# Kernel tuning notes

Measured on AMD Instinct MI355X. Metric: run time of the kernel, lower is better.

The kernel has to match this reference:

```python
import jax, jax.numpy as jnp
import numpy as np

B = 65536      # batch
E = 4          # experts per node
F = 32         # per-node input features
H = 256        # hidden width
NODES = 4
D_MID = 128    # intermediate node output dim
D_OUT = 8      # final head dim


def _lin_w(k, fan_in, fan_out):
    b = 1.0 / np.sqrt(fan_in)
    return jax.random.uniform(k, (E, fan_in, fan_out), jnp.float32, -b, b)


def setup_inputs() -> dict:
    key = jax.random.key(0)
    ks = jax.random.split(key, 8)
    feats = jax.random.normal(ks[0], (B, NODES * F), dtype=jnp.float32)
    # routing one-hot blocks embedded in the input vector (as the module expects)
    ohs = [jax.nn.one_hot(jax.random.randint(ks[1 + j], (B,), 0, E), E, dtype=jnp.float32)
           for j in range(NODES)]
    input_val = jnp.concatenate([feats] + ohs, axis=1)  # [B, 144]
    p = {"input_val": input_val}
    kc = iter(jax.random.split(ks[5], 32))
    # node 0: no pre-interface; post: F->H relu, H->D_MID relu
    p["W0_0"] = _lin_w(next(kc), F, H); p["b0_0"] = jnp.full((E, H), 0.1, jnp.float32)
    p["W0_1"] = _lin_w(next(kc), H, D_MID); p["b0_1"] = jnp.full((E, D_MID), 0.1, jnp.float32)
    # nodes 1,2: pre F->H relu; post (D_MID+H)->H relu, H->D_MID relu
    for j in (1, 2):
        p[f"W{j}_pre"] = _lin_w(next(kc), F, H); p[f"b{j}_pre"] = jnp.full((E, H), 0.1, jnp.float32)
        p[f"W{j}_0"] = _lin_w(next(kc), D_MID + H, H); p[f"b{j}_0"] = jnp.full((E, H), 0.1, jnp.float32)
        p[f"W{j}_1"] = _lin_w(next(kc), H, D_MID); p[f"b{j}_1"] = jnp.full((E, D_MID), 0.1, jnp.float32)
    # node 3 (output): pre F->H relu; post (D_MID+H)->H relu, H->D_OUT identity
    p["W3_pre"] = _lin_w(next(kc), F, H); p["b3_pre"] = jnp.full((E, H), 0.1, jnp.float32)
    p["W3_0"] = _lin_w(next(kc), D_MID + H, H); p["b3_0"] = jnp.full((E, H), 0.1, jnp.float32)
    p["W3_1"] = jax.random.uniform(next(kc), (E, H, D_OUT), jnp.float32, -0.003, 0.003)
    p["b3_1"] = jax.random.uniform(next(kc), (E, D_OUT), jnp.float32, -0.003, 0.003)
    return p


def reference(input_val, W0_0, b0_0, W0_1, b0_1,
              W1_pre, b1_pre, W1_0, b1_0, W1_1, b1_1,
              W2_pre, b2_pre, W2_0, b2_0, W2_1, b2_1,
              W3_pre, b3_pre, W3_0, b3_0, W3_1, b3_1):
    relu = jax.nn.relu
    xs = [input_val[:, j * F:(j + 1) * F] for j in range(NODES)]          # per-node features
    ohs = [input_val[:, NODES * F + j * E: NODES * F + (j + 1) * E] for j in range(NODES)]

    def combine(oh, outs):  # oh [B,E] exact one-hot; outs [E,B,D] -> exact per-row expert pick
        return jnp.einsum('be,ebo->bo', oh, outs)

    # node 0 (no previous-level input)
    def n0(W0, b0, W1, b1):
        h = relu(xs[0] @ W0 + b0)
        return relu(h @ W1 + b1)
    x = combine(ohs[0], jax.vmap(n0)(W0_0, b0_0, W0_1, b0_1))  # [B, D_MID]

    def node(xj, xprev, relu_last):
        def f(Wp, bp, W0, b0, W1, b1):
            h = relu(xj @ Wp + bp)                      # pre-interface
            h = jnp.concatenate([xprev, h], axis=-1)    # interface: cat(prev, pre)
            h = relu(h @ W0 + b0)
            o = h @ W1 + b1
            return relu(o) if relu_last else o
        return f

    x = combine(ohs[1], jax.vmap(node(xs[1], x, True))(W1_pre, b1_pre, W1_0, b1_0, W1_1, b1_1))
    x = combine(ohs[2], jax.vmap(node(xs[2], x, True))(W2_pre, b2_pre, W2_0, b2_0, W2_1, b2_1))
    x = combine(ohs[3], jax.vmap(node(xs[3], x, False))(W3_pre, b3_pre, W3_0, b3_0, W3_1, b3_1))
    return x  # [B, D_OUT]
```

## Files before the change

### kernel.cpp

```cpp
#include <hip/hip_runtime.h>
#include <hip/hip_bf16.h>
#include <stdint.h>

typedef unsigned int u32;
typedef unsigned short u16;
typedef unsigned char u8;
typedef __bf16 bf16x8 __attribute__((ext_vector_type(8)));
typedef float f32x4 __attribute__((ext_vector_type(4)));

#define NB 65536
#define NBLK 1280
#define PERM_TOT (NBLK * 64)
#define INVR 0xFFFFFFFFu
#define BLK_DEAD 0xFFFFu

#define O_ROWS 0
#define O_XJ   256
#define O_P    (O_XJ + 4096)
#define O_H    (O_P + 16384)
#define O_RED  O_P
#define SM_BYTES (O_H + 32768)

__device__ __host__ constexpr int TS(int m) {
  constexpr int t[12] = {0, 64, 320, 384, 1152, 1408, 1472, 2240, 2496, 2560, 3328, 3360};
  return t[m];
}

__device__ __forceinline__ u16 f2bf(float f) {
  u32 u = __builtin_bit_cast(u32, f);
  u32 r = (u + 0x7FFFu + ((u >> 16) & 1u)) >> 16;
  return (u16)r;
}
__device__ __forceinline__ u32 cvtpk(float lo, float hi) {
  u32 r;
  asm("v_cvt_pk_bf16_f32 %0, %1, %2" : "=v"(r) : "v"(lo), "v"(hi));
  return r;
}
__device__ __forceinline__ float relu_f(float x) { return x > 0.f ? x : 0.f; }
__device__ __forceinline__ f32x4 mfma16(bf16x8 a, bf16x8 b, f32x4 c) {
  return __builtin_amdgcn_mfma_f32_16x16x32_bf16(a, b, c, 0, 0, 0);
}

__device__ __forceinline__ void mkpair(f32x4 acc, float bias, bool dorelu, int l16,
                                       u32& w0, u32& w1) {
  float v0 = acc[0] + bias, v1 = acc[1] + bias, v2 = acc[2] + bias, v3 = acc[3] + bias;
  if (dorelu) { v0 = relu_f(v0); v1 = relu_f(v1); v2 = relu_f(v2); v3 = relu_f(v3); }
  u32 a = cvtpk(v0, v1);
  u32 b = cvtpk(v2, v3);
  u32 ax = (u32)__shfl_xor((int)a, 1);
  u32 bx = (u32)__shfl_xor((int)b, 1);
  if ((l16 & 1) == 0) { w0 = (a & 0xffffu) | (ax << 16); w1 = (a >> 16) | (ax & 0xffff0000u); }
  else                { w0 = (bx & 0xffffu) | (b << 16); w1 = (bx >> 16) | (b & 0xffff0000u); }
}

__device__ __forceinline__ void frag_store_pair(char* base, int KT, int m0, int col,
                                                u32 w0, u32 w1) {
  char* d = base + (((m0 >> 4) * KT + (col >> 5)) << 10) +
            (((m0 & 15) + (((col & 31) >> 3) << 4)) << 4) + (col & 7) * 2;
  *(u32*)d = w0; *(u32*)(d + 16) = w1;
}


struct PrepArgs {
  const float* src[11];
  int K[11], Nsrc[11];
  int tileStart[12];
};

__device__ __forceinline__ void prep_tile_dev(__bf16* __restrict__ pk, const PrepArgs& pa,
                                              int gt, int lane) {
  const int quad = lane >> 4, l16 = lane & 15;
  int m = 0;
  while (gt >= pa.tileStart[m + 1]) m++;
  const int loc = gt - pa.tileStart[m];
  const int K = pa.K[m], Ns = pa.Nsrc[m];
  const int Np = Ns < 16 ? 16 : Ns;
  const int KT = K >> 5, NT = Np >> 4;
  const int e = loc / (KT * NT), rem = loc % (KT * NT);
  const int nt = rem / KT, kt = rem % KT;
  const int k = kt * 32 + quad * 8, n = nt * 16 + l16;
  u32 hw[4];
  if (n < Ns) {
    const float* s = pa.src[m] + ((size_t)e * K + k) * Ns + n;
    u16 h[8];
#pragma unroll
    for (int j = 0; j < 8; j++) h[j] = f2bf(s[(size_t)j * Ns]);
    hw[0] = (u32)h[0] | ((u32)h[1] << 16);
    hw[1] = (u32)h[2] | ((u32)h[3] << 16);
    hw[2] = (u32)h[4] | ((u32)h[5] << 16);
    hw[3] = (u32)h[6] | ((u32)h[7] << 16);
  } else {
    hw[0] = hw[1] = hw[2] = hw[3] = 0u;
  }
  uint4 w; w.x = hw[0]; w.y = hw[1]; w.z = hw[2]; w.w = hw[3];
  *(uint4*)((char*)pk + (size_t)gt * 1024 + lane * 16) = w;
}


__global__ __launch_bounds__(256) void k_front(const float* __restrict__ inp,
                                               u8* __restrict__ bkt,
                                               u32* __restrict__ cnt2,
                                               u32* __restrict__ rank,
                                               __bf16* __restrict__ pk, PrepArgs pa) {
  __shared__ u32 h[256];
  const int tid = threadIdx.x;
  if (blockIdx.x == 0) rank[tid] = 0u;
  h[tid] = 0u;
  __syncthreads();
  const int r = blockIdx.x * 256 + tid;
  const float4* oh = (const float4*)(inp + (size_t)r * 144 + 128);
  u32 b = 0;
#pragma unroll
  for (int j = 0; j < 4; j++) {
    float4 v = oh[j];
    u32 e = v.y > 0.5f ? 1u : (v.z > 0.5f ? 2u : (v.w > 0.5f ? 3u : 0u));
    b |= e << (2 * j);
  }
  bkt[r] = (u8)b;
  atomicAdd(&h[b], 1u);
  __syncthreads();
  cnt2[blockIdx.x * 256 + tid] = h[tid];
  for (int g4 = blockIdx.x; g4 < TS(11) / 4; g4 += 256)
    prep_tile_dev(pk, pa, g4 * 4 + (tid >> 6), tid & 63);
}


__global__ __launch_bounds__(256) void k_place(const u8* __restrict__ bkt,
                                               const u32* __restrict__ cnt2,
                                               u32* __restrict__ rank,
                                               u16* __restrict__ blk2b,
                                               u32* __restrict__ perm) {
  __shared__ u32 s[256], base[256];
  const int tid = threadIdx.x;
  u32 c = 0;
#pragma unroll 8
  for (int j = 0; j < 256; j++) c += cnt2[j * 256 + tid];
  const u32 pad = (c + 63u) & ~63u;
  s[tid] = pad;
  __syncthreads();
  for (int d = 1; d < 256; d <<= 1) {
    u32 v = (tid >= d) ? s[tid - d] : 0u;
    __syncthreads();
    s[tid] += v;
    __syncthreads();
  }
  const u32 off = s[tid] - pad;
  const u32 total = s[255];
  __syncthreads();
  if (blockIdx.x == 0) {
    for (u32 i = off + c; i < off + pad; i++) perm[i] = INVR;
    for (u32 blk = off >> 6; blk < (off + pad) >> 6; blk++) blk2b[blk] = (u16)tid;
    for (u32 blk = (total >> 6) + tid; blk < NBLK; blk += 256) blk2b[blk] = BLK_DEAD;
  }
  s[tid] = 0u;
  __syncthreads();
  const int r = blockIdx.x * 256 + tid;
  const u32 b = bkt[r];
  const u32 lrk = atomicAdd(&s[b], 1u);
  __syncthreads();
  base[tid] = off + (s[tid] ? atomicAdd(&rank[tid], s[tid]) : 0u);
  __syncthreads();
  perm[base[b] + lrk] = (u32)r;
}


__device__ __forceinline__ void xj_load(const float* inp, u32 myrow, int tid, int node,
                                        float4& v0, float4& v1) {
  v0 = make_float4(0.f, 0.f, 0.f, 0.f); v1 = v0;
  if (tid < 256 && myrow != INVR) {
    const int c8 = (tid & 3) << 3;
    const float4* p = (const float4*)(inp + (size_t)myrow * 144 + node * 32 + c8);
    v0 = p[0]; v1 = p[1];
  }
}

__device__ __forceinline__ void xj_store(char* sm, int tid, float4 v0, float4 v1) {
  if (tid >= 256) return;
  const int r = tid >> 2;
  uint4 w;
  w.x = cvtpk(v0.x, v0.y);
  w.y = cvtpk(v0.z, v0.w);
  w.z = cvtpk(v1.x, v1.y);
  w.w = cvtpk(v1.z, v1.w);
  *(uint4*)(sm + O_XJ + ((r >> 4) << 10) + ((((tid & 3) << 4) + (r & 15)) << 4)) = w;
}

__device__ __forceinline__ void pre_gemm(char* sm, u32 e, int wave, int lane,
                                         const __bf16* Wp, const float* bp) {
  const int l16 = lane & 15;
  const int wn0 = wave * 32;
  const int rsel = ((lane >> 4) << 2) + ((l16 & 1) ? 2 : 0);
  const int colp = l16 & ~1;
  float bias[2];
#pragma unroll
  for (int nt = 0; nt < 2; nt++) bias[nt] = bp[(size_t)e * 256 + wn0 + nt * 16 + l16];
  f32x4 acc[4][2];
#pragma unroll
  for (int i = 0; i < 4; i++) { acc[i][0] = (f32x4){0.f,0.f,0.f,0.f}; acc[i][1] = acc[i][0]; }
  bf16x8 a[4], b[2];
#pragma unroll
  for (int nt = 0; nt < 2; nt++)
    b[nt] = *(const bf16x8*)(Wp + (size_t)(e * 16 + (wn0 >> 4) + nt) * 512 + lane * 8);
#pragma unroll
  for (int mt = 0; mt < 4; mt++)
    a[mt] = *(const bf16x8*)(sm + O_XJ + (mt << 10) + lane * 16);
#pragma unroll
  for (int mt = 0; mt < 4; mt++)
#pragma unroll
    for (int nt = 0; nt < 2; nt++) acc[mt][nt] = mfma16(a[mt], b[nt], acc[mt][nt]);
#pragma unroll
  for (int nt = 0; nt < 2; nt++) {
    const int n = wn0 + nt * 16;
#pragma unroll
    for (int mt = 0; mt < 4; mt++) {
      u32 w0, w1;
      mkpair(acc[mt][nt], bias[nt], true, l16, w0, w1);
      frag_store_pair(sm + O_H, 8, mt * 16 + rsel, n + colp, w0, w1);
    }
  }
}

__device__ __forceinline__ void main_gemm(char* sm, u32 e, int wave, int lane,
                                          const __bf16* Wm, const float* bm) {
  const int l16 = lane & 15;
  const int wn0 = wave * 32;
  const int rsel = ((lane >> 4) << 2) + ((l16 & 1) ? 2 : 0);
  const int colp = l16 & ~1;
  float bias[2];
#pragma unroll
  for (int nt = 0; nt < 2; nt++) bias[nt] = bm[(size_t)e * 256 + wn0 + nt * 16 + l16];
  f32x4 acc[4][2];
#pragma unroll
  for (int i = 0; i < 4; i++) { acc[i][0] = (f32x4){0.f,0.f,0.f,0.f}; acc[i][1] = acc[i][0]; }
  const __bf16* bB = Wm + (size_t)(e * 16 + (wn0 >> 4)) * 12 * 512 + lane * 8;
  bf16x8 bb[2][2];
#pragma unroll
  for (int nt = 0; nt < 2; nt++) {
    bb[0][nt] = *(const bf16x8*)(bB + (size_t)(nt * 12 + 0) * 512);
    bb[1][nt] = *(const bf16x8*)(bB + (size_t)(nt * 12 + 1) * 512);
  }
#pragma unroll
  for (int kt = 0; kt < 12; kt++) {
    bf16x8 a[4];
#pragma unroll
    for (int mt = 0; mt < 4; mt++) {
      a[mt] = (kt < 4)
          ? *(const bf16x8*)(sm + O_P + ((mt * 4 + kt) << 10) + lane * 16)
          : *(const bf16x8*)(sm + O_H + ((mt * 8 + (kt - 4)) << 10) + lane * 16);
    }
#pragma unroll
    for (int mt = 0; mt < 4; mt++)
#pragma unroll
      for (int nt = 0; nt < 2; nt++) acc[mt][nt] = mfma16(a[mt], bb[kt & 1][nt], acc[mt][nt]);
    if (kt < 10) {
#pragma unroll
      for (int nt = 0; nt < 2; nt++)
        bb[kt & 1][nt] = *(const bf16x8*)(bB + (size_t)(nt * 12 + kt + 2) * 512);
    }
  }
  __syncthreads();
#pragma unroll
  for (int nt = 0; nt < 2; nt++) {
    const int n = wn0 + nt * 16;
#pragma unroll
    for (int mt = 0; mt < 4; mt++) {
      u32 w0, w1;
      mkpair(acc[mt][nt], bias[nt], true, l16, w0, w1);
      frag_store_pair(sm + O_H, 8, mt * 16 + rsel, n + colp, w0, w1);
    }
  }
  __syncthreads();
}

__device__ __forceinline__ void out_gemm(char* sm, u32 e, int wave, int lane,
                                         const __bf16* Wo, const float* bo) {
  const int l16 = lane & 15;
  const int on0 = wave * 16;
  const int rsel = ((lane >> 4) << 2) + ((l16 & 1) ? 2 : 0);
  const int colp = l16 & ~1;
  const float bias0 = bo[(size_t)e * 128 + on0 + l16];
  f32x4 acc[4];
#pragma unroll
  for (int i = 0; i < 4; i++) acc[i] = (f32x4){0.f, 0.f, 0.f, 0.f};
  const __bf16* bB = Wo + (size_t)(e * 8 + (on0 >> 4)) * 8 * 512 + lane * 8;
  bf16x8 bb[2];
  bb[0] = *(const bf16x8*)(bB);
  bb[1] = *(const bf16x8*)(bB + 512);
#pragma unroll
  for (int kt = 0; kt < 8; kt++) {
    bf16x8 a[4];
#pragma unroll
    for (int mt = 0; mt < 4; mt++)
      a[mt] = *(const bf16x8*)(sm + O_H + ((mt * 8 + kt) << 10) + lane * 16);
#pragma unroll
    for (int mt = 0; mt < 4; mt++) acc[mt] = mfma16(a[mt], bb[kt & 1], acc[mt]);
    if (kt < 6) bb[kt & 1] = *(const bf16x8*)(bB + (size_t)(kt + 2) * 512);
  }
#pragma unroll
  for (int mt = 0; mt < 4; mt++) {
    u32 w0, w1;
    mkpair(acc[mt], bias0, true, l16, w0, w1);
    frag_store_pair(sm + O_P, 4, mt * 16 + rsel, on0 + colp, w0, w1);
  }
}

__global__ __launch_bounds__(512, 6) void fused_k(
    const float* __restrict__ inp, const u32* __restrict__ perm,
    const u16* __restrict__ blk2b, const __bf16* __restrict__ pk,
    const float* __restrict__ b0_0, const float* __restrict__ b0_1,
    const float* __restrict__ b1_p, const float* __restrict__ b1_0,
    const float* __restrict__ b1_1, const float* __restrict__ b2_p,
    const float* __restrict__ b2_0, const float* __restrict__ b2_1,
    const float* __restrict__ b3_p, const float* __restrict__ b3_0,
    const float* __restrict__ b3_1, float* __restrict__ dout) {
  const u32 b = blk2b[blockIdx.x];
  if (b == BLK_DEAD) return;
  __shared__ __align__(16) char sm[SM_BYTES];
  u32* rows = (u32*)sm;
  const int tid = threadIdx.x;
  const int wave = tid >> 6, lane = tid & 63, quad = lane >> 4, l16 = lane & 15;
  if (tid < 64) rows[tid] = perm[blockIdx.x * 64 + tid];
  const u32 e0 = b & 3u, e1 = (b >> 2) & 3u, e2 = (b >> 4) & 3u, e3 = (b >> 6) & 3u;
  __syncthreads();
  const u32 myrow = rows[(tid & 255) >> 2];

  float4 v0, v1;
  xj_load(inp, myrow, tid, 0, v0, v1);
  xj_store(sm, tid, v0, v1);
  __syncthreads();
  pre_gemm(sm, e0, wave, lane, pk + (size_t)TS(0) * 512, b0_0);
  __syncthreads();
  xj_load(inp, myrow, tid, 1, v0, v1);
  out_gemm(sm, e0, wave, lane, pk + (size_t)TS(1) * 512, b0_1);
  xj_store(sm, tid, v0, v1);
  __syncthreads();
  pre_gemm(sm, e1, wave, lane, pk + (size_t)TS(2) * 512, b1_p);
  __syncthreads();
  main_gemm(sm, e1, wave, lane, pk + (size_t)TS(3) * 512, b1_0);
  xj_load(inp, myrow, tid, 2, v0, v1);
  out_gemm(sm, e1, wave, lane, pk + (size_t)TS(4) * 512, b1_1);
  xj_store(sm, tid, v0, v1);
  __syncthreads();
  pre_gemm(sm, e2, wave, lane, pk + (size_t)TS(5) * 512, b2_p);
  __syncthreads();
  main_gemm(sm, e2, wave, lane, pk + (size_t)TS(6) * 512, b2_0);
  xj_load(inp, myrow, tid, 3, v0, v1);
  out_gemm(sm, e2, wave, lane, pk + (size_t)TS(7) * 512, b2_1);
  xj_store(sm, tid, v0, v1);
  __syncthreads();
  pre_gemm(sm, e3, wave, lane, pk + (size_t)TS(8) * 512, b3_p);
  __syncthreads();
  main_gemm(sm, e3, wave, lane, pk + (size_t)TS(9) * 512, b3_0);

  {
    const __bf16* Wo3 = pk + (size_t)TS(10) * 512;
    if (wave < 4) {
      f32x4 acc3[4];
#pragma unroll
      for (int i = 0; i < 4; i++) acc3[i] = (f32x4){0.f, 0.f, 0.f, 0.f};
#pragma unroll
      for (int kk = 0; kk < 2; kk++) {
        const int kt = wave * 2 + kk;
        bf16x8 b3 = *(const bf16x8*)(Wo3 + (size_t)(e3 * 8 + kt) * 512 + lane * 8);
        bf16x8 a[4];
#pragma unroll
        for (int mt = 0; mt < 4; mt++)
          a[mt] = *(const bf16x8*)(sm + O_H + ((mt * 8 + kt) << 10) + lane * 16);
#pragma unroll
        for (int mt = 0; mt < 4; mt++) acc3[mt] = mfma16(a[mt], b3, acc3[mt]);
      }
#pragma unroll
      for (int mt = 0; mt < 4; mt++)
#pragma unroll
        for (int r = 0; r < 4; r++)
          *(float*)(sm + O_RED +
                    (((size_t)wave * 64 + mt * 16 + quad * 4 + r) * 16 + l16) * 4) = acc3[mt][r];
    }
    __syncthreads();
    if (tid < 256) {
      const int m = tid >> 2, c = (tid & 3) * 2;
      float s0 = 0.f, s1 = 0.f;
#pragma unroll
      for (int w = 0; w < 4; w++) {
        s0 += *(float*)(sm + O_RED + (((size_t)w * 64 + m) * 16 + c) * 4);
        s1 += *(float*)(sm + O_RED + (((size_t)w * 64 + m) * 16 + c + 1) * 4);
      }
      if (myrow != INVR) {
        float2 o;
        o.x = s0 + b3_1[(size_t)e3 * 8 + c];
        o.y = s1 + b3_1[(size_t)e3 * 8 + c + 1];
        *(float2*)(dout + (size_t)myrow * 8 + c) = o;
      }
    }
  }
}


extern "C" void kernel_launch(void* const* d_in, const int* in_sizes, int n_in,
                              void* d_out, int out_size, void* d_ws, size_t ws_size,
                              hipStream_t stream) {
  (void)in_sizes; (void)n_in; (void)out_size; (void)ws_size;
  const float* inp = (const float*)d_in[0];
  char* ws = (char*)d_ws;

  const size_t oBKT = 0;
  const size_t oRANK = oBKT + NB;
  const size_t oB2B = oRANK + 1024;
  const size_t oCNT2 = (oB2B + NBLK * 2 + 255) & ~(size_t)255;
  const size_t oPERM = oCNT2 + 256 * 256 * 4;
  const size_t oPK = (oPERM + (size_t)PERM_TOT * 4 + 255) & ~(size_t)255;

  u8* bkt = (u8*)(ws + oBKT);
  u32* rank = (u32*)(ws + oRANK);
  u16* blk2b = (u16*)(ws + oB2B);
  u32* cnt2 = (u32*)(ws + oCNT2);
  u32* perm = (u32*)(ws + oPERM);
  __bf16* pk = (__bf16*)(ws + oPK);

  PrepArgs pa;
  const int widx[11] = {1, 3, 5, 7, 9, 11, 13, 15, 17, 19, 21};
  const int Ks[11] = {32, 256, 32, 384, 256, 32, 384, 256, 32, 384, 256};
  const int Ns[11] = {256, 128, 256, 256, 128, 256, 256, 128, 256, 256, 8};
  for (int m = 0; m < 11; m++) {
    pa.src[m] = (const float*)d_in[widx[m]];
    pa.K[m] = Ks[m]; pa.Nsrc[m] = Ns[m]; pa.tileStart[m] = TS(m);
  }
  pa.tileStart[11] = TS(11);

  hipLaunchKernelGGL(k_front, dim3(NB / 256), dim3(256), 0, stream,
                     inp, bkt, cnt2, rank, pk, pa);
  hipLaunchKernelGGL(k_place, dim3(NB / 256), dim3(256), 0, stream,
                     bkt, cnt2, rank, blk2b, perm);
  fused_k<<<NBLK, 512, 0, stream>>>(
      inp, perm, blk2b, pk,
      (const float*)d_in[2], (const float*)d_in[4],
      (const float*)d_in[6], (const float*)d_in[8], (const float*)d_in[10],
      (const float*)d_in[12], (const float*)d_in[14], (const float*)d_in[16],
      (const float*)d_in[18], (const float*)d_in[20], (const float*)d_in[22],
      (float*)d_out);
}
```

Measured before the change: 215.3 us.

## Pre-convert features to bf16 in front kernel and stage via direct global-to-LDS loads

The front kernel now converts all 128 feature columns of every row to bf16 and writes them to a workspace buffer. The fused kernel then copies each node's 32-column slice straight into shared memory with global_load_lds, run by four waves, in place of fp32 loads followed by register conversion and LDS stores. This halves the bytes gathered per row in the main kernel and removes the conversion and store instructions from its critical path. The cost is an extra full pass over the input plus a write of a B×128 bf16 buffer in the front kernel.

```diff
diff --git a/kernel.cpp b/kernel.cpp
--- a/kernel.cpp
+++ b/kernel.cpp
@@ -101,6 +101,7 @@
                                                u8* __restrict__ bkt,
                                                u32* __restrict__ cnt2,
                                                u32* __restrict__ rank,
+                                               u32* __restrict__ fb_u32,
                                                __bf16* __restrict__ pk, PrepArgs pa) {
   __shared__ u32 h[256];
   const int tid = threadIdx.x;
@@ -120,6 +121,15 @@
   atomicAdd(&h[b], 1u);
   __syncthreads();
   cnt2[blockIdx.x * 256 + tid] = h[tid];
+#pragma unroll 4
+  for (int it = 0; it < 32; it++) {
+    const int cg = it * 256 + tid;
+    const int lrow = cg >> 5, c4 = cg & 31;
+    const size_t grow = (size_t)blockIdx.x * 256 + lrow;
+    float4 v = *(const float4*)(inp + grow * 144 + c4 * 4);
+    uint2 o; o.x = cvtpk(v.x, v.y); o.y = cvtpk(v.z, v.w);
+    *(uint2*)(fb_u32 + grow * 64 + c4 * 2) = o;
+  }
   for (int g4 = blockIdx.x; g4 < TS(11) / 4; g4 += 256)
     prep_tile_dev(pk, pa, g4 * 4 + (tid >> 6), tid & 63);
 }
@@ -164,25 +174,14 @@
 }
 
 
-__device__ __forceinline__ void xj_load(const float* inp, u32 myrow, int tid, int node,
-                                        float4& v0, float4& v1) {
-  v0 = make_float4(0.f, 0.f, 0.f, 0.f); v1 = v0;
-  if (tid < 256 && myrow != INVR) {
-    const int c8 = (tid & 3) << 3;
-    const float4* p = (const float4*)(inp + (size_t)myrow * 144 + node * 32 + c8);
-    v0 = p[0]; v1 = p[1];
-  }
-}
-
-__device__ __forceinline__ void xj_store(char* sm, int tid, float4 v0, float4 v1) {
-  if (tid >= 256) return;
-  const int r = tid >> 2;
-  uint4 w;
-  w.x = cvtpk(v0.x, v0.y);
-  w.y = cvtpk(v0.z, v0.w);
-  w.z = cvtpk(v1.x, v1.y);
-  w.w = cvtpk(v1.z, v1.w);
-  *(uint4*)(sm + O_XJ + ((r >> 4) << 10) + ((((tid & 3) << 4) + (r & 15)) << 4)) = w;
+__device__ __forceinline__ void xj_stage(char* sm, const __bf16* fbsrc, int node,
+                                         int wave) {
+  if (wave < 4) {
+    __builtin_amdgcn_global_load_lds(
+        (const __attribute__((address_space(1))) void*)(fbsrc + node * 32),
+        (__attribute__((address_space(3))) void*)(sm + O_XJ + (wave << 10)),
+        16, 0, 0);
+  }
 }
 
 __device__ __forceinline__ void pre_gemm(char* sm, u32 e, int wave, int lane,
@@ -305,7 +304,7 @@
 }
 
 __global__ __launch_bounds__(512, 6) void fused_k(
-    const float* __restrict__ inp, const u32* __restrict__ perm,
+    const __bf16* __restrict__ fb, const u32* __restrict__ perm,
     const u16* __restrict__ blk2b, const __bf16* __restrict__ pk,
     const float* __restrict__ b0_0, const float* __restrict__ b0_1,
     const float* __restrict__ b1_p, const float* __restrict__ b1_0,
@@ -322,31 +321,31 @@
   if (tid < 64) rows[tid] = perm[blockIdx.x * 64 + tid];
   const u32 e0 = b & 3u, e1 = (b >> 2) & 3u, e2 = (b >> 4) & 3u, e3 = (b >> 6) & 3u;
   __syncthreads();
-  const u32 myrow = rows[(tid & 255) >> 2];
-
-  float4 v0, v1;
-  xj_load(inp, myrow, tid, 0, v0, v1);
-  xj_store(sm, tid, v0, v1);
+  const __bf16* fbsrc = fb;
+  if (wave < 4) {
+    u32 srow = rows[(wave << 4) + l16];
+    if (srow == INVR) srow = 0;
+    fbsrc = fb + (size_t)srow * 128 + (lane >> 4) * 8;
+  }
+
+  xj_stage(sm, fbsrc, 0, wave);
   __syncthreads();
   pre_gemm(sm, e0, wave, lane, pk + (size_t)TS(0) * 512, b0_0);
   __syncthreads();
-  xj_load(inp, myrow, tid, 1, v0, v1);
+  xj_stage(sm, fbsrc, 1, wave);
   out_gemm(sm, e0, wave, lane, pk + (size_t)TS(1) * 512, b0_1);
-  xj_store(sm, tid, v0, v1);
   __syncthreads();
   pre_gemm(sm, e1, wave, lane, pk + (size_t)TS(2) * 512, b1_p);
   __syncthreads();
   main_gemm(sm, e1, wave, lane, pk + (size_t)TS(3) * 512, b1_0);
-  xj_load(inp, myrow, tid, 2, v0, v1);
+  xj_stage(sm, fbsrc, 2, wave);
   out_gemm(sm, e1, wave, lane, pk + (size_t)TS(4) * 512, b1_1);
-  xj_store(sm, tid, v0, v1);
   __syncthreads();
   pre_gemm(sm, e2, wave, lane, pk + (size_t)TS(5) * 512, b2_p);
   __syncthreads();
   main_gemm(sm, e2, wave, lane, pk + (size_t)TS(6) * 512, b2_0);
-  xj_load(inp, myrow, tid, 3, v0, v1);
+  xj_stage(sm, fbsrc, 3, wave);
   out_gemm(sm, e2, wave, lane, pk + (size_t)TS(7) * 512, b2_1);
-  xj_store(sm, tid, v0, v1);
   __syncthreads();
   pre_gemm(sm, e3, wave, lane, pk + (size_t)TS(8) * 512, b3_p);
   __syncthreads();
@@ -385,6 +384,7 @@
         s0 += *(float*)(sm + O_RED + (((size_t)w * 64 + m) * 16 + c) * 4);
         s1 += *(float*)(sm + O_RED + (((size_t)w * 64 + m) * 16 + c + 1) * 4);
       }
+      const u32 myrow = rows[m];
       if (myrow != INVR) {
         float2 o;
         o.x = s0 + b3_1[(size_t)e3 * 8 + c];
@@ -403,13 +403,15 @@
   const float* inp = (const float*)d_in[0];
   char* ws = (char*)d_ws;
 
-  const size_t oBKT = 0;
+  const size_t oFB = 0;
+  const size_t oBKT = oFB + (size_t)NB * 256;
   const size_t oRANK = oBKT + NB;
   const size_t oB2B = oRANK + 1024;
   const size_t oCNT2 = (oB2B + NBLK * 2 + 255) & ~(size_t)255;
   const size_t oPERM = oCNT2 + 256 * 256 * 4;
   const size_t oPK = (oPERM + (size_t)PERM_TOT * 4 + 255) & ~(size_t)255;
 
+  __bf16* fb = (__bf16*)(ws + oFB);
   u8* bkt = (u8*)(ws + oBKT);
   u32* rank = (u32*)(ws + oRANK);
   u16* blk2b = (u16*)(ws + oB2B);
@@ -428,11 +430,11 @@
   pa.tileStart[11] = TS(11);
 
   hipLaunchKernelGGL(k_front, dim3(NB / 256), dim3(256), 0, stream,
-                     inp, bkt, cnt2, rank, pk, pa);
+                     inp, bkt, cnt2, rank, (u32*)fb, pk, pa);
   hipLaunchKernelGGL(k_place, dim3(NB / 256), dim3(256), 0, stream,
                      bkt, cnt2, rank, blk2b, perm);
   fused_k<<<NBLK, 512, 0, stream>>>(
-      inp, perm, blk2b, pk,
+      fb, perm, blk2b, pk,
       (const float*)d_in[2], (const float*)d_in[4],
       (const float*)d_in[6], (const float*)d_in[8], (const float*)d_in[10],
       (const float*)d_in[12], (const float*)d_in[14], (const float*)d_in[16],
```

Result: slower. 225.8 us (+4.9%).

## Specialize waves: half load next-node inputs, half compute output GEMM

Applied to the files above, without the earlier changes.

Splits the eight waves into two roles at each node boundary. Waves 0-3 load and convert the next node's input features into shared memory. Waves 4-7 compute the 128-wide output GEMM, with each wave now covering 32 columns instead of 16. The intent is to overlap global-memory input loads with MFMA work on separate waves instead of having every wave do both in sequence. The cost is that the GEMM runs on half the waves with more accumulators per wave, which raises register pressure and lengthens that phase.

```diff
diff --git a/kernel.cpp b/kernel.cpp
--- a/kernel.cpp
+++ b/kernel.cpp
@@ -167,7 +167,7 @@
 __device__ __forceinline__ void xj_load(const float* inp, u32 myrow, int tid, int node,
                                         float4& v0, float4& v1) {
   v0 = make_float4(0.f, 0.f, 0.f, 0.f); v1 = v0;
-  if (tid < 256 && myrow != INVR) {
+  if (myrow != INVR) {
     const int c8 = (tid & 3) << 3;
     const float4* p = (const float4*)(inp + (size_t)myrow * 144 + node * 32 + c8);
     v0 = p[0]; v1 = p[1];
@@ -175,7 +175,6 @@
 }
 
 __device__ __forceinline__ void xj_store(char* sm, int tid, float4 v0, float4 v1) {
-  if (tid >= 256) return;
   const int r = tid >> 2;
   uint4 w;
   w.x = cvtpk(v0.x, v0.y);
@@ -272,20 +271,25 @@
   __syncthreads();
 }
 
-__device__ __forceinline__ void out_gemm(char* sm, u32 e, int wave, int lane,
+__device__ __forceinline__ void out_gemm(char* sm, u32 e, int wv2, int lane,
                                          const __bf16* Wo, const float* bo) {
   const int l16 = lane & 15;
-  const int on0 = wave * 16;
+  const int on0 = wv2 * 32;
   const int rsel = ((lane >> 4) << 2) + ((l16 & 1) ? 2 : 0);
   const int colp = l16 & ~1;
-  const float bias0 = bo[(size_t)e * 128 + on0 + l16];
-  f32x4 acc[4];
-#pragma unroll
-  for (int i = 0; i < 4; i++) acc[i] = (f32x4){0.f, 0.f, 0.f, 0.f};
+  float bias[2];
+#pragma unroll
+  for (int nt = 0; nt < 2; nt++) bias[nt] = bo[(size_t)e * 128 + on0 + nt * 16 + l16];
+  f32x4 acc[4][2];
+#pragma unroll
+  for (int i = 0; i < 4; i++) { acc[i][0] = (f32x4){0.f,0.f,0.f,0.f}; acc[i][1] = acc[i][0]; }
   const __bf16* bB = Wo + (size_t)(e * 8 + (on0 >> 4)) * 8 * 512 + lane * 8;
-  bf16x8 bb[2];
-  bb[0] = *(const bf16x8*)(bB);
-  bb[1] = *(const bf16x8*)(bB + 512);
+  bf16x8 bb[2][2];
+#pragma unroll
+  for (int nt = 0; nt < 2; nt++) {
+    bb[0][nt] = *(const bf16x8*)(bB + (size_t)(nt * 8 + 0) * 512);
+    bb[1][nt] = *(const bf16x8*)(bB + (size_t)(nt * 8 + 1) * 512);
+  }
 #pragma unroll
   for (int kt = 0; kt < 8; kt++) {
     bf16x8 a[4];
@@ -293,14 +297,24 @@
     for (int mt = 0; mt < 4; mt++)
       a[mt] = *(const bf16x8*)(sm + O_H + ((mt * 8 + kt) << 10) + lane * 16);
 #pragma unroll
-    for (int mt = 0; mt < 4; mt++) acc[mt] = mfma16(a[mt], bb[kt & 1], acc[mt]);
-    if (kt < 6) bb[kt & 1] = *(const bf16x8*)(bB + (size_t)(kt + 2) * 512);
-  }
-#pragma unroll
-  for (int mt = 0; mt < 4; mt++) {
-    u32 w0, w1;
-    mkpair(acc[mt], bias0, true, l16, w0, w1);
-    frag_store_pair(sm + O_P, 4, mt * 16 + rsel, on0 + colp, w0, w1);
+    for (int mt = 0; mt < 4; mt++)
+#pragma unroll
+      for (int nt = 0; nt < 2; nt++) acc[mt][nt] = mfma16(a[mt], bb[kt & 1][nt], acc[mt][nt]);
+    if (kt < 6) {
+#pragma unroll
+      for (int nt = 0; nt < 2; nt++)
+        bb[kt & 1][nt] = *(const bf16x8*)(bB + (size_t)(nt * 8 + kt + 2) * 512);
+    }
+  }
+#pragma unroll
+  for (int nt = 0; nt < 2; nt++) {
+    const int n = on0 + nt * 16;
+#pragma unroll
+    for (int mt = 0; mt < 4; mt++) {
+      u32 w0, w1;
+      mkpair(acc[mt][nt], bias[nt], true, l16, w0, w1);
+      frag_store_pair(sm + O_P, 4, mt * 16 + rsel, n + colp, w0, w1);
+    }
   }
 }
 
@@ -325,28 +339,39 @@
   const u32 myrow = rows[(tid & 255) >> 2];
 
   float4 v0, v1;
-  xj_load(inp, myrow, tid, 0, v0, v1);
-  xj_store(sm, tid, v0, v1);
+  if (wave < 4) {
+    xj_load(inp, myrow, tid, 0, v0, v1);
+    xj_store(sm, tid, v0, v1);
+  }
   __syncthreads();
   pre_gemm(sm, e0, wave, lane, pk + (size_t)TS(0) * 512, b0_0);
   __syncthreads();
-  xj_load(inp, myrow, tid, 1, v0, v1);
-  out_gemm(sm, e0, wave, lane, pk + (size_t)TS(1) * 512, b0_1);
-  xj_store(sm, tid, v0, v1);
+  if (wave < 4) {
+    xj_load(inp, myrow, tid, 1, v0, v1);
+    xj_store(sm, tid, v0, v1);
+  } else {
+    out_gemm(sm, e0, wave - 4, lane, pk + (size_t)TS(1) * 512, b0_1);
+  }
   __syncthreads();
   pre_gemm(sm, e1, wave, lane, pk + (size_t)TS(2) * 512, b1_p);
   __syncthreads();
   main_gemm(sm, e1, wave, lane, pk + (size_t)TS(3) * 512, b1_0);
-  xj_load(inp, myrow, tid, 2, v0, v1);
-  out_gemm(sm, e1, wave, lane, pk + (size_t)TS(4) * 512, b1_1);
-  xj_store(sm, tid, v0, v1);
+  if (wave < 4) {
+    xj_load(inp, myrow, tid, 2, v0, v1);
+    xj_store(sm, tid, v0, v1);
+  } else {
+    out_gemm(sm, e1, wave - 4, lane, pk + (size_t)TS(4) * 512, b1_1);
+  }
   __syncthreads();
   pre_gemm(sm, e2, wave, lane, pk + (size_t)TS(5) * 512, b2_p);
   __syncthreads();
   main_gemm(sm, e2, wave, lane, pk + (size_t)TS(6) * 512, b2_0);
-  xj_load(inp, myrow, tid, 3, v0, v1);
-  out_gemm(sm, e2, wave, lane, pk + (size_t)TS(7) * 512, b2_1);
-  xj_store(sm, tid, v0, v1);
+  if (wave < 4) {
+    xj_load(inp, myrow, tid, 3, v0, v1);
+    xj_store(sm, tid, v0, v1);
+  } else {
+    out_gemm(sm, e2, wave - 4, lane, pk + (size_t)TS(7) * 512, b2_1);
+  }
   __syncthreads();
   pre_gemm(sm, e3, wave, lane, pk + (size_t)TS(8) * 512, b3_p);
   __syncthreads();
```

Measured after the change: 220.4 us. 2.4% more time.
